# Optimization experiments

Hardware: AMD Instinct MI355X
Metric: run time of the kernel (lower is better)

## Reference

```python
import jax, jax.numpy as jnp
import numpy as np

C, H, K, G = 256, 8, 32, 8
HD = C // H
SCALE = HD ** -0.5
POS_BND = int(0.8 * K * 1 ** 0.5)  # 25
RPE_NUM = 2 * POS_BND + 1          # 51
NW = 4096


def setup_inputs() -> dict:
    key = jax.random.key(0)
    ks = jax.random.split(key, 8)
    data = jax.random.normal(ks[0], (NW * (K + G), C), dtype=jnp.float32)
    # relative xyz offsets between points in a window; exercise the clamp
    rel_pos = jax.random.randint(ks[1], (NW, K, K, 3), -POS_BND - 5, POS_BND + 6).astype(jnp.int32)
    # additive mask: 0 for valid pairs, -100 for masked (padded) pairs
    keep = jax.random.bernoulli(ks[2], 0.9, (NW, K + G, K + G))
    mask = jnp.where(keep, 0.0, -100.0).astype(jnp.float32)
    qkv_w = jax.random.normal(ks[3], (C, 3 * C), dtype=jnp.float32) * (C ** -0.5)
    qkv_b = jnp.zeros((3 * C,), dtype=jnp.float32)
    proj_w = jax.random.normal(ks[4], (C, C), dtype=jnp.float32) * (C ** -0.5)
    proj_b = jnp.zeros((C,), dtype=jnp.float32)
    rpe_table = jax.random.normal(ks[5], (3 * RPE_NUM, H), dtype=jnp.float32) * 0.02
    return {"data": data, "rel_pos": rel_pos, "mask": mask, "qkv_w": qkv_w,
            "qkv_b": qkv_b, "proj_w": proj_w, "proj_b": proj_b, "rpe_table": rpe_table}


def reference(data, rel_pos, mask, qkv_w, qkv_b, proj_w, proj_b, rpe_table):
    W = K + G  # window size including context tokens
    qkv = data @ qkv_w + qkv_b                              # (T, 3C)
    qkv_std = jnp.std(qkv, axis=0, ddof=1)                  # torch .std is unbiased
    qkv = qkv.reshape(-1, W, 3, H, HD).transpose(2, 0, 3, 1, 4)  # (3, Nw, H, W, HD)
    q, k, v = qkv[0] * SCALE, qkv[1], qkv[2]
    attn = jnp.einsum('nhqd,nhkd->nhqk', q, k)              # (Nw, H, W, W)
    # RPE: clamp offsets, index per-axis slices of table, sum over xyz
    idx = jnp.clip(rel_pos, -POS_BND, POS_BND) + POS_BND + jnp.arange(3, dtype=rel_pos.dtype) * RPE_NUM
    rpe = rpe_table[idx].sum(axis=3)                        # (Nw, K, K, H)
    rpe = rpe.transpose(0, 3, 1, 2)                         # (Nw, H, K, K)
    rpe = jnp.pad(rpe, ((0, 0), (0, 0), (G, 0), (G, 0)))    # pad for context tokens
    attn = attn + rpe + mask[:, None]
    attn = jax.nn.softmax(attn, axis=-1)
    out = jnp.einsum('nhqk,nhkd->nqhd', attn, v).reshape(-1, W, C)
    out = out @ proj_w + proj_b                             # (Nw, W, C)
    return (out, qkv_std)
```

## Files before the change

kernel.cpp:

```cpp
#include <hip/hip_runtime.h>
#include <math.h>

#define SCALE_F 0.17677669529663687f

typedef __bf16 bf16x8 __attribute__((ext_vector_type(8)));
typedef float f32x4 __attribute__((ext_vector_type(4)));

__device__ __forceinline__ unsigned short f2bf(float f) {
  unsigned u = __builtin_bit_cast(unsigned, f);
  u = (u + 0x7FFFu + ((u >> 16) & 1u)) >> 16;
  return (unsigned short)u;
}
__device__ __forceinline__ float bf2f(unsigned short u) {
  return __builtin_bit_cast(float, (unsigned)u << 16);
}
__device__ __forceinline__ unsigned pk2(float a, float b) {
  return (unsigned)f2bf(a) | ((unsigned)f2bf(b) << 16);
}
__device__ __forceinline__ bf16x8 ld16(const void* p) {
  int4 v = *(const int4*)p;
  return __builtin_bit_cast(bf16x8, v);
}
__device__ __forceinline__ void gll16(const void* g, void* l) {
  __builtin_amdgcn_global_load_lds(
      (const __attribute__((address_space(1))) unsigned int*)g,
      (__attribute__((address_space(3))) unsigned int*)l, 16, 0, 0);
}


__global__ void octa_prep2(const float* __restrict__ qkv_w, const float* __restrict__ proj_w,
                           unsigned short* __restrict__ wTq, unsigned short* __restrict__ pTq)
{
  int e = blockIdx.x * 256 + threadIdx.x;
  if (e < 196608) {
    int c = e >> 13;
    int nc = c >> 3, kc = c & 7;
    int p2 = e & 8191;
    int n = p2 >> 5, cw = p2 & 31;
    int kl = cw ^ (((n >> 1) & 3) << 3);
    wTq[e] = f2bf(qkv_w[(size_t)(kc * 32 + kl) * 768 + nc * 256 + n]);
  } else {
    int e2 = e - 196608;
    int kc = e2 >> 13, p2 = e2 & 8191;
    int n = p2 >> 5, cw = p2 & 31;
    int kl = cw ^ (((n >> 1) & 3) << 3);
    pTq[e2] = f2bf(proj_w[(size_t)(kc * 32 + kl) * 256 + n]);
  }
}

#define KQ_A0 0
#define KQ_A1 8192
#define KQ_B0 16384
#define KQ_B1 32768
#define KQ_LDS 49152

__global__ __launch_bounds__(512, 4)
void octa_qkv(const float* __restrict__ data, const float* __restrict__ qkv_b,
              const unsigned short* __restrict__ wTq, float* __restrict__ ws,
              char* __restrict__ qg, char* __restrict__ kg, char* __restrict__ vg)
{
  extern __shared__ char smem[];
  const int tid = threadIdx.x, lane = tid & 63, wid = tid >> 6;
  const int ql = lane & 15, lg = lane >> 4;
  const int bm = blockIdx.x / 3, nc = blockIdx.x - bm * 3;
  const int wr = wid >> 2, wc = wid & 3;
  const char* wbase = (const char*)wTq + (size_t)nc * 131072;

  const int arow = tid >> 2, aq = tid & 3;
  const float* abase = data + ((size_t)bm * 128 + arow) * 256 + aq * 8;
  const int alds = arow * 64 + ((aq * 16) ^ (((arow >> 1) & 3) << 4));

  float4 a0 = *(const float4*)abase;
  float4 a1 = *(const float4*)(abase + 4);
  gll16(wbase + wid * 1024 + lane * 16, smem + KQ_B0 + wid * 1024);
  gll16(wbase + 8192 + wid * 1024 + lane * 16, smem + KQ_B0 + 8192 + wid * 1024);
  *(uint2*)(smem + KQ_A0 + alds) = make_uint2(pk2(a0.x, a0.y), pk2(a0.z, a0.w));
  *(uint2*)(smem + KQ_A0 + alds + 8) = make_uint2(pk2(a1.x, a1.y), pk2(a1.z, a1.w));
  __syncthreads();

  f32x4 acc[4][4];
  #pragma unroll
  for (int m = 0; m < 4; ++m)
    #pragma unroll
    for (int n = 0; n < 4; ++n) acc[m][n] = (f32x4){0.f, 0.f, 0.f, 0.f};

  #pragma unroll
  for (int t = 0; t < 8; ++t) {
    float4 na0, na1;
    if (t < 7) {
      na0 = *(const float4*)(abase + (t + 1) * 32);
      na1 = *(const float4*)(abase + (t + 1) * 32 + 4);
      const char* bsrc = wbase + (size_t)(t + 1) * 16384;
      char* bb1 = smem + (((t + 1) & 1) ? KQ_B1 : KQ_B0);
      gll16(bsrc + wid * 1024 + lane * 16, bb1 + wid * 1024);
      gll16(bsrc + 8192 + wid * 1024 + lane * 16, bb1 + 8192 + wid * 1024);
    }
    const char* ab = smem + ((t & 1) ? KQ_A1 : KQ_A0);
    const char* bb = smem + ((t & 1) ? KQ_B1 : KQ_B0);
    bf16x8 af[4], bf[4];
    #pragma unroll
    for (int mt = 0; mt < 4; ++mt) {
      int row = wr * 64 + mt * 16 + ql;
      af[mt] = ld16(ab + row * 64 + ((lg * 16) ^ (((row >> 1) & 3) << 4)));
    }
    #pragma unroll
    for (int nt = 0; nt < 4; ++nt) {
      int n = wc * 64 + nt * 16 + ql;
      bf[nt] = ld16(bb + n * 64 + ((lg * 16) ^ (((n >> 1) & 3) << 4)));
    }
    #pragma unroll
    for (int nt = 0; nt < 4; ++nt)
      #pragma unroll
      for (int mt = 0; mt < 4; ++mt)
        acc[mt][nt] = __builtin_amdgcn_mfma_f32_16x16x32_bf16(af[mt], bf[nt], acc[mt][nt], 0, 0, 0);
    if (t < 7) {
      char* ab1 = smem + (((t + 1) & 1) ? KQ_A1 : KQ_A0);
      *(uint2*)(ab1 + alds) = make_uint2(pk2(na0.x, na0.y), pk2(na0.z, na0.w));
      *(uint2*)(ab1 + alds + 8) = make_uint2(pk2(na1.x, na1.y), pk2(na1.z, na1.w));
    }
    __syncthreads();
  }

  char* base = nc == 0 ? qg : (nc == 1 ? kg : vg);
  const float cs = (nc == 0) ? SCALE_F : 1.0f;
  #pragma unroll
  for (int nt = 0; nt < 4; ++nt) {
    int col = wc * 64 + nt * 16 + ql;
    int h = col >> 5, d = col & 31;
    float bias = qkv_b[nc * 256 + col];
    float s1 = 0.f, s2 = 0.f;
    #pragma unroll
    for (int mt = 0; mt < 4; ++mt) {
      int tg0 = bm * 128 + wr * 64 + mt * 16 + lg * 4;
      int w = tg0 / 40, tk0 = tg0 - w * 40;
      size_t slice = (size_t)(w * 8 + h) * 2560;
      #pragma unroll
      for (int r = 0; r < 4; ++r) {
        float v = acc[mt][nt][r] + bias;
        s1 += v; s2 += v * v;
        *(unsigned short*)(base + slice + (tk0 + r) * 64 + d * 2) = f2bf(v * cs);
      }
    }
    s1 += __shfl_xor(s1, 16); s1 += __shfl_xor(s1, 32);
    s2 += __shfl_xor(s2, 16); s2 += __shfl_xor(s2, 32);
    if (lg == 0) {
      atomicAdd(ws + nc * 256 + col, s1);
      atomicAdd(ws + 768 + nc * 256 + col, s2);
    }
  }
}

#define F3_LDS 30720

__global__ __launch_bounds__(512, 4)
void octa_attnproj3(const char* __restrict__ qg, const char* __restrict__ kg,
                    const char* __restrict__ vg, const float* __restrict__ maskp,
                    const int* __restrict__ rel_pos, const float* __restrict__ rpe_table,
                    const unsigned short* __restrict__ pTq, const float* __restrict__ proj_b,
                    float* __restrict__ out)
{
  extern __shared__ char smem[];
  const int tid = threadIdx.x, w = blockIdx.x, wid = tid >> 6;
  const int lane = tid & 63, ql = lane & 15, lg = lane >> 4, h = wid;
  const int perm = ql * 64 + lg * 16;
  const char* qb = qg + (size_t)(w * 8 + h) * 2560;
  const char* kb = kg + (size_t)(w * 8 + h) * 2560;
  const char* vb = vg + (size_t)(w * 8 + h) * 2560;

  bf16x8 kf0 = ld16(kb + perm), kf1 = ld16(kb + 1024 + perm), kf2 = ld16(kb + 2048 + perm);
  bf16x8 qf0 = ld16(qb + perm), qf1 = ld16(qb + 1024 + perm), qf2 = ld16(qb + 2048 + perm);
  union U8 { unsigned short u[8]; bf16x8 v; };
  U8 ua, ub, uc, ud;
  #pragma unroll
  for (int j = 0; j < 8; ++j) {
    int tok = lg * 8 + j;
    ua.u[j] = *(const unsigned short*)(vb + tok * 64 + ql * 2);
    ub.u[j] = *(const unsigned short*)(vb + tok * 64 + (16 + ql) * 2);
  }
  if (lg == 0) {
    #pragma unroll
    for (int j = 0; j < 8; ++j) {
      uc.u[j] = *(const unsigned short*)(vb + (32 + j) * 64 + ql * 2);
      ud.u[j] = *(const unsigned short*)(vb + (32 + j) * 64 + (16 + ql) * 2);
    }
  } else {
    #pragma unroll
    for (int j = 0; j < 8; ++j) { uc.u[j] = 0; ud.u[j] = 0; }
  }
  bf16x8 vA = ua.v, vB = ub.v, vC = uc.v, vD = ud.v;

  for (int e = tid; e < 1600; e += 512) {
    int qi = e / 40, kj = e - qi * 40;
    float m = maskp[(size_t)w * 1600 + e];
    float b8[8];
    if (qi >= 8 && kj >= 8) {
      const int* rp = rel_pos + ((size_t)w * 1024 + (qi - 8) * 32 + (kj - 8)) * 3;
      int c0 = rp[0], c1 = rp[1], c2 = rp[2];
      c0 = min(25, max(-25, c0)); c1 = min(25, max(-25, c1)); c2 = min(25, max(-25, c2));
      const float4* r0 = (const float4*)(rpe_table + (c0 + 25) * 8);
      const float4* r1 = (const float4*)(rpe_table + (c1 + 76) * 8);
      const float4* r2 = (const float4*)(rpe_table + (c2 + 127) * 8);
      float4 a0 = r0[0], a1 = r1[0], a2 = r2[0];
      float4 b0 = r0[1], b1 = r1[1], b2 = r2[1];
      b8[0] = m + a0.x + a1.x + a2.x; b8[1] = m + a0.y + a1.y + a2.y;
      b8[2] = m + a0.z + a1.z + a2.z; b8[3] = m + a0.w + a1.w + a2.w;
      b8[4] = m + b0.x + b1.x + b2.x; b8[5] = m + b0.y + b1.y + b2.y;
      b8[6] = m + b0.z + b1.z + b2.z; b8[7] = m + b0.w + b1.w + b2.w;
    } else {
      #pragma unroll
      for (int hh = 0; hh < 8; ++hh) b8[hh] = m;
    }
    #pragma unroll
    for (int hh = 0; hh < 8; ++hh)
      *(unsigned short*)(smem + hh * 3200 + kj * 80 + qi * 2) = f2bf(b8[hh]);
  }

  f32x4 st[9];
  {
    bf16x8 kf[3] = {kf0, kf1, kf2}, qf[3] = {qf0, qf1, qf2};
    __builtin_amdgcn_s_setprio(1);
    #pragma unroll
    for (int a = 0; a < 3; ++a)
      #pragma unroll
      for (int b = 0; b < 3; ++b)
        st[a * 3 + b] = __builtin_amdgcn_mfma_f32_16x16x32_bf16(
            kf[a], qf[b], (f32x4){0.f, 0.f, 0.f, 0.f}, 0, 0, 0);
    __builtin_amdgcn_s_setprio(0);
  }
  __syncthreads();

  const char* bb_ = smem + h * 3200;
  float mx[3] = {-3e38f, -3e38f, -3e38f};
  #pragma unroll
  for (int a = 0; a < 3; ++a) {
    #pragma unroll
    for (int b = 0; b < 3; ++b) {
      #pragma unroll
      for (int r = 0; r < 4; ++r) {
        int kj = a * 16 + lg * 4 + r;
        int qi = b * 16 + ql;
        float s = st[a * 3 + b][r];
        if (kj < 40) {
          if (qi < 40)
            s += bf2f(*(const unsigned short*)(bb_ + kj * 80 + qi * 2));
        } else {
          s = -1e30f;
        }
        st[a * 3 + b][r] = s;
        mx[b] = fmaxf(mx[b], s);
      }
    }
  }
  __syncthreads();

  #pragma unroll
  for (int b = 0; b < 3; ++b) {
    mx[b] = fmaxf(mx[b], __shfl_xor(mx[b], 16));
    mx[b] = fmaxf(mx[b], __shfl_xor(mx[b], 32));
  }
  float sum[3] = {0.f, 0.f, 0.f};
  #pragma unroll
  for (int a = 0; a < 3; ++a)
    #pragma unroll
    for (int b = 0; b < 3; ++b)
      #pragma unroll
      for (int r = 0; r < 4; ++r) {
        float e = __expf(st[a * 3 + b][r] - mx[b]);
        st[a * 3 + b][r] = e;
        sum[b] += e;
      }
  float inv[3];
  #pragma unroll
  for (int b = 0; b < 3; ++b) {
    sum[b] += __shfl_xor(sum[b], 16);
    sum[b] += __shfl_xor(sum[b], 32);
    inv[b] = 1.f / sum[b];
  }

  char* pb_ = smem + wid * 3840;
  f32x4 ot[6];
  #pragma unroll
  for (int i = 0; i < 6; ++i) ot[i] = (f32x4){0.f, 0.f, 0.f, 0.f};

  #pragma unroll
  for (int a = 0; a < 2; ++a)
    #pragma unroll
    for (int b = 0; b < 3; ++b)
      #pragma unroll
      for (int r = 0; r < 4; ++r) {
        int kj = a * 16 + lg * 4 + r, qi = b * 16 + ql;
        *(unsigned short*)(pb_ + qi * 80 + kj * 2) = f2bf(st[a * 3 + b][r] * inv[b]);
      }
  asm volatile("" ::: "memory");
  __builtin_amdgcn_s_setprio(1);
  #pragma unroll
  for (int b = 0; b < 3; ++b) {
    bf16x8 pf = ld16(pb_ + (b * 16 + ql) * 80 + lg * 16);
    ot[b]     = __builtin_amdgcn_mfma_f32_16x16x32_bf16(vA, pf, ot[b], 0, 0, 0);
    ot[3 + b] = __builtin_amdgcn_mfma_f32_16x16x32_bf16(vB, pf, ot[3 + b], 0, 0, 0);
  }
  __builtin_amdgcn_s_setprio(0);
  asm volatile("" ::: "memory");
  #pragma unroll
  for (int b = 0; b < 3; ++b) {
    int qi = b * 16 + ql;
    #pragma unroll
    for (int r = 0; r < 4; ++r)
      *(unsigned short*)(pb_ + qi * 80 + (lg * 4 + r) * 2) = f2bf(st[6 + b][r] * inv[b]);
    *(uint2*)(pb_ + qi * 80 + 32 + lg * 8) = make_uint2(0u, 0u);
  }
  asm volatile("" ::: "memory");
  __builtin_amdgcn_s_setprio(1);
  #pragma unroll
  for (int b = 0; b < 3; ++b) {
    bf16x8 pf = ld16(pb_ + (b * 16 + ql) * 80 + lg * 16);
    ot[b]     = __builtin_amdgcn_mfma_f32_16x16x32_bf16(vC, pf, ot[b], 0, 0, 0);
    ot[3 + b] = __builtin_amdgcn_mfma_f32_16x16x32_bf16(vD, pf, ot[3 + b], 0, 0, 0);
  }
  __builtin_amdgcn_s_setprio(0);

  __syncthreads();
  #pragma unroll
  for (int dm = 0; dm < 2; ++dm)
    #pragma unroll
    for (int b = 0; b < 3; ++b) {
      int qi = b * 16 + ql;
      unsigned u0 = pk2(ot[dm * 3 + b][0], ot[dm * 3 + b][1]);
      unsigned u1 = pk2(ot[dm * 3 + b][2], ot[dm * 3 + b][3]);
      int colb = (h * 32 + dm * 16 + lg * 4) * 2;
      *(uint2*)(smem + qi * 512 + (colb ^ ((qi & 7) << 4))) = make_uint2(u0, u1);
    }
  __syncthreads();

  f32x4 pacc[3][2];
  #pragma unroll
  for (int m = 0; m < 3; ++m)
    #pragma unroll
    for (int n = 0; n < 2; ++n) pacc[m][n] = (f32x4){0.f, 0.f, 0.f, 0.f};
  const int c0 = wid * 32;
  const char* pB = (const char*)pTq;

  #pragma unroll
  for (int t = 0; t < 8; ++t) {
    bf16x8 af[3], bfr[2];
    #pragma unroll
    for (int mt = 0; mt < 3; ++mt) {
      int row = mt * 16 + ql;
      af[mt] = ld16(smem + row * 512 + ((t * 64 + lg * 16) ^ ((row & 7) << 4)));
    }
    #pragma unroll
    for (int nt = 0; nt < 2; ++nt) {
      int n = c0 + nt * 16 + ql;
      bfr[nt] = ld16(pB + (size_t)t * 16384 + n * 64 + ((lg * 16) ^ (((n >> 1) & 3) << 4)));
    }
    __builtin_amdgcn_s_setprio(1);
    #pragma unroll
    for (int nt = 0; nt < 2; ++nt)
      #pragma unroll
      for (int mt = 0; mt < 3; ++mt)
        pacc[mt][nt] = __builtin_amdgcn_mfma_f32_16x16x32_bf16(af[mt], bfr[nt], pacc[mt][nt], 0, 0, 0);
    __builtin_amdgcn_s_setprio(0);
  }

  #pragma unroll
  for (int nt = 0; nt < 2; ++nt) {
    int col = c0 + nt * 16 + ql;
    float pb = proj_b[col];
    #pragma unroll
    for (int mt = 0; mt < 3; ++mt)
      #pragma unroll
      for (int r = 0; r < 4; ++r) {
        int row = mt * 16 + lg * 4 + r;
        if (row < 40)
          out[(size_t)(w * 40 + row) * 256 + col] = pacc[mt][nt][r] + pb;
      }
  }
}

__global__ void octa_std(const float* __restrict__ ws, float* __restrict__ out,
                         int total_rows, size_t off)
{
  int j = blockIdx.x * 256 + threadIdx.x;
  if (j < 768) {
    float s = ws[j], ss = ws[768 + j];
    float T = (float)total_rows;
    float var = (ss - s * s / T) / (T - 1.f);
    out[off + j] = sqrtf(fmaxf(var, 0.f));
  }
}

#define O_RPE 0
#define O_MSK 4896
#define O_IDX 8096
#define O_A   12192
#define O_ATT 36768
#define B1_SZ 49152
#define ATT_STRIDE 11776
#define AK 3840
#define AV 7680
#define B2_S (O_ATT + 94208)
#define B2_A O_ATT
#define LDS_BYTES_V4 163744

__device__ __forceinline__ int a_addr(int row, int byte) {
  return O_A + row * 512 + (byte ^ ((row & 7) << 4));
}
__device__ __forceinline__ int v_addr(int d, int byte) {
  return AV + d * 128 + (byte ^ ((d & 7) << 4));
}

__global__ void octa_prep_v4(const float* __restrict__ qkv_w, const float* __restrict__ proj_w,
                             unsigned short* __restrict__ wTq, unsigned short* __restrict__ pTq)
{
  int idx = blockIdx.x * 256 + threadIdx.x;
  if (idx < 196608) {
    int n = idx >> 8, k = idx & 255;
    wTq[idx] = f2bf(qkv_w[k * 768 + n]);
  } else {
    int i = idx - 196608;
    int n = i >> 8, k = i & 255;
    pTq[i] = f2bf(proj_w[k * 256 + n]);
  }
}

__global__ __launch_bounds__(512, 2)
void octa_main_v4(const float* __restrict__ data, const int* __restrict__ rel_pos,
                  const float* __restrict__ maskp, const float* __restrict__ qkv_b,
                  const float* __restrict__ proj_b, const float* __restrict__ rpe_table,
                  const unsigned short* __restrict__ wTq, const unsigned short* __restrict__ pTq,
                  float* __restrict__ ws, float* __restrict__ out)
{
  extern __shared__ char smem[];
  float* s_rpe = (float*)(smem + O_RPE);
  const int tid = threadIdx.x;
  const int w   = blockIdx.x;
  const int wid = tid >> 6;
  const int lane = tid & 63;
  const int ql = lane & 15;
  const int lg = lane >> 4;
  const int h  = wid;
  const int ab = O_ATT + wid * ATT_STRIDE;

  {
    #pragma unroll
    for (int it = 0; it < 6; ++it) {
      int g = it * 512 + tid;
      int n = g >> 2, slot = g & 3;
      const char* src = (const char*)wTq + (size_t)n * 512 + ((slot * 16) ^ ((n & 3) << 4));
      gll16(src, smem + O_ATT + it * 8192 + wid * 1024);
    }
  }
  for (int f = tid; f < 1224; f += 512) s_rpe[f] = rpe_table[f];
  for (int f = tid; f < 400; f += 512) {
    float4 m4 = ((const float4*)(maskp + (size_t)w * 1600))[f];
    uint2 pk;
    pk.x = pk2(m4.x, m4.y); pk.y = pk2(m4.z, m4.w);
    *(uint2*)(smem + O_MSK + f * 8) = pk;
  }
  for (int p = tid; p < 1024; p += 512) {
    const int* rp = rel_pos + ((size_t)w * 1024 + p) * 3;
    int c0 = rp[0], c1 = rp[1], c2 = rp[2];
    c0 = min(25, max(-25, c0)); c1 = min(25, max(-25, c1)); c2 = min(25, max(-25, c2));
    unsigned pk = (unsigned)(c0 + 25) | ((unsigned)(c1 + 76) << 10) | ((unsigned)(c2 + 127) << 20);
    *(unsigned*)(smem + O_IDX + ((p * 4) ^ (((p >> 5) & 7) << 4))) = pk;
  }
  {
    const float4* src = (const float4*)(data + (size_t)w * 10240);
    for (int f = tid; f < 2560; f += 512) {
      int token = f >> 6, q4 = f & 63;
      float4 d4 = src[f];
      uint2 pk;
      pk.x = pk2(d4.x, d4.y); pk.y = pk2(d4.z, d4.w);
      *(uint2*)(smem + a_addr(token, q4 * 8)) = pk;
    }
    int token = 40 + (tid >> 6), byte = (tid & 63) * 8;
    *(uint2*)(smem + a_addr(token, byte)) = make_uint2(0u, 0u);
  }
  __syncthreads();

  f32x4 acc[18];
  #pragma unroll
  for (int i = 0; i < 18; ++i) acc[i] = (f32x4){0.f, 0.f, 0.f, 0.f};

  for (int t = 0; t < 8; ++t) {
    if (t < 7) {
      int bb = O_ATT + ((t + 1) & 1) * B1_SZ;
      #pragma unroll
      for (int it = 0; it < 6; ++it) {
        int g = it * 512 + tid;
        int n = g >> 2, slot = g & 3;
        const char* src = (const char*)wTq + (size_t)n * 512 + (t + 1) * 64
                          + ((slot * 16) ^ ((n & 3) << 4));
        gll16(src, smem + bb + it * 8192 + wid * 1024);
      }
    }
    const int bb = O_ATT + (t & 1) * B1_SZ;
    bf16x8 af[3];
    #pragma unroll
    for (int mt = 0; mt < 3; ++mt)
      af[mt] = ld16(smem + a_addr(mt * 16 + ql, t * 64 + lg * 16));
    #pragma unroll
    for (int j = 0; j < 6; ++j) {
      int n = ((j >> 1) * 16 + 2 * wid + (j & 1)) * 16 + ql;
      bf16x8 bf = ld16(smem + bb + n * 64 + ((lg * 16) ^ ((n & 3) << 4)));
      #pragma unroll
      for (int mt = 0; mt < 3; ++mt)
        acc[j * 3 + mt] = __builtin_amdgcn_mfma_f32_16x16x32_bf16(af[mt], bf, acc[j * 3 + mt], 0, 0, 0);
    }
    __syncthreads();
  }

  {
    #pragma unroll
    for (int it = 0; it < 4; ++it) {
      int g = it * 512 + tid;
      int n = g >> 3, slot = g & 7;
      const char* src = (const char*)pTq + (size_t)n * 512 + ((slot * 16) ^ ((n & 7) << 4));
      gll16(src, smem + B2_S + it * 8192 + wid * 1024);
    }
  }

  #pragma unroll
  for (int j = 0; j < 6; ++j) {
    int sec = j >> 1;
    int ncol = sec * 256 + 32 * wid + (j & 1) * 16 + ql;
    int d = (j & 1) * 16 + ql;
    float bias = qkv_b[ncol];
    float s1 = 0.f, s2 = 0.f;
    #pragma unroll
    for (int mt = 0; mt < 3; ++mt) {
      #pragma unroll
      for (int r = 0; r < 4; ++r) {
        int token = mt * 16 + lg * 4 + r;
        float v = acc[j * 3 + mt][r] + bias;
        if (token < 40) { s1 += v; s2 += v * v; }
        if (sec == 0)
          *(unsigned short*)(smem + ab + token * 80 + d * 2) = f2bf(v * SCALE_F);
        else if (sec == 1)
          *(unsigned short*)(smem + ab + AK + token * 80 + d * 2) = f2bf(v);
        else
          *(unsigned short*)(smem + ab + v_addr(d, token * 2)) = f2bf(v);
      }
    }
    s1 += __shfl_xor(s1, 16); s1 += __shfl_xor(s1, 32);
    s2 += __shfl_xor(s2, 16); s2 += __shfl_xor(s2, 32);
    if (lg == 0) { atomicAdd(ws + ncol, s1); atomicAdd(ws + 768 + ncol, s2); }
  }
  {
    int zd = lane >> 1;
    int zb = 96 + (lane & 1) * 16;
    *(int4*)(smem + ab + v_addr(zd, zb)) = (int4){0, 0, 0, 0};
  }
  asm volatile("" ::: "memory");

  f32x4 st[9];
  {
    bf16x8 kf[3], qf[3];
    #pragma unroll
    for (int a = 0; a < 3; ++a) kf[a] = ld16(smem + ab + AK + (a * 16 + ql) * 80 + lg * 16);
    #pragma unroll
    for (int b = 0; b < 3; ++b) qf[b] = ld16(smem + ab + (b * 16 + ql) * 80 + lg * 16);
    #pragma unroll
    for (int a = 0; a < 3; ++a)
      #pragma unroll
      for (int b = 0; b < 3; ++b)
        st[a * 3 + b] = __builtin_amdgcn_mfma_f32_16x16x32_bf16(
            kf[a], qf[b], (f32x4){0.f, 0.f, 0.f, 0.f}, 0, 0, 0);
  }

  float mx[3] = {-3e38f, -3e38f, -3e38f};
  #pragma unroll
  for (int a = 0; a < 3; ++a) {
    #pragma unroll
    for (int b = 0; b < 3; ++b) {
      #pragma unroll
      for (int r = 0; r < 4; ++r) {
        int kj = a * 16 + lg * 4 + r;
        int qi = b * 16 + ql;
        float s = st[a * 3 + b][r];
        if (kj < 40) {
          if (qi < 40) {
            s += bf2f(*(const unsigned short*)(smem + O_MSK + (qi * 40 + kj) * 2));
            if (kj >= 8 && qi >= 8) {
              int p = (qi - 8) * 32 + (kj - 8);
              unsigned pk = *(const unsigned*)(smem + O_IDX + ((p * 4) ^ (((p >> 5) & 7) << 4)));
              s += s_rpe[(pk & 1023) * 8 + h] + s_rpe[((pk >> 10) & 1023) * 8 + h]
                 + s_rpe[(pk >> 20) * 8 + h];
            }
          }
        } else {
          s = -1e30f;
        }
        st[a * 3 + b][r] = s;
        mx[b] = fmaxf(mx[b], s);
      }
    }
  }
  #pragma unroll
  for (int b = 0; b < 3; ++b) {
    mx[b] = fmaxf(mx[b], __shfl_xor(mx[b], 16));
    mx[b] = fmaxf(mx[b], __shfl_xor(mx[b], 32));
  }
  float sum[3] = {0.f, 0.f, 0.f};
  #pragma unroll
  for (int a = 0; a < 3; ++a)
    #pragma unroll
    for (int b = 0; b < 3; ++b)
      #pragma unroll
      for (int r = 0; r < 4; ++r) {
        float e = __expf(st[a * 3 + b][r] - mx[b]);
        st[a * 3 + b][r] = e;
        sum[b] += e;
      }
  float inv[3];
  #pragma unroll
  for (int b = 0; b < 3; ++b) {
    sum[b] += __shfl_xor(sum[b], 16);
    sum[b] += __shfl_xor(sum[b], 32);
    inv[b] = 1.f / sum[b];
  }

  f32x4 ot[6];
  #pragma unroll
  for (int i = 0; i < 6; ++i) ot[i] = (f32x4){0.f, 0.f, 0.f, 0.f};

  #pragma unroll
  for (int a = 0; a < 2; ++a)
    #pragma unroll
    for (int b = 0; b < 3; ++b)
      #pragma unroll
      for (int r = 0; r < 4; ++r) {
        int kj = a * 16 + lg * 4 + r, qi = b * 16 + ql;
        *(unsigned short*)(smem + ab + qi * 80 + kj * 2) = f2bf(st[a * 3 + b][r] * inv[b]);
      }
  asm volatile("" ::: "memory");
  {
    bf16x8 vf0 = ld16(smem + ab + v_addr(ql, lg * 16));
    bf16x8 vf1 = ld16(smem + ab + v_addr(16 + ql, lg * 16));
    #pragma unroll
    for (int b = 0; b < 3; ++b) {
      bf16x8 pf = ld16(smem + ab + (b * 16 + ql) * 80 + lg * 16);
      ot[b] = __builtin_amdgcn_mfma_f32_16x16x32_bf16(vf0, pf, ot[b], 0, 0, 0);
      ot[3 + b] = __builtin_amdgcn_mfma_f32_16x16x32_bf16(vf1, pf, ot[3 + b], 0, 0, 0);
    }
  }
  asm volatile("" ::: "memory");
  #pragma unroll
  for (int b = 0; b < 3; ++b) {
    int qi = b * 16 + ql;
    #pragma unroll
    for (int r = 0; r < 4; ++r) {
      int kj = 32 + lg * 4 + r;
      *(unsigned short*)(smem + ab + qi * 80 + (kj - 32) * 2) = f2bf(st[6 + b][r] * inv[b]);
    }
    *(uint2*)(smem + ab + qi * 80 + 32 + lg * 8) = make_uint2(0u, 0u);
  }
  asm volatile("" ::: "memory");
  {
    bf16x8 vf0 = ld16(smem + ab + v_addr(ql, 64 + lg * 16));
    bf16x8 vf1 = ld16(smem + ab + v_addr(16 + ql, 64 + lg * 16));
    #pragma unroll
    for (int b = 0; b < 3; ++b) {
      bf16x8 pf = ld16(smem + ab + (b * 16 + ql) * 80 + lg * 16);
      ot[b] = __builtin_amdgcn_mfma_f32_16x16x32_bf16(vf0, pf, ot[b], 0, 0, 0);
      ot[3 + b] = __builtin_amdgcn_mfma_f32_16x16x32_bf16(vf1, pf, ot[3 + b], 0, 0, 0);
    }
  }
  #pragma unroll
  for (int dm = 0; dm < 2; ++dm)
    #pragma unroll
    for (int b = 0; b < 3; ++b)
      #pragma unroll
      for (int r = 0; r < 4; ++r) {
        int d = dm * 16 + lg * 4 + r;
        int qi = b * 16 + ql;
        *(unsigned short*)(smem + a_addr(qi, (h * 32 + d) * 2)) = f2bf(ot[dm * 3 + b][r]);
      }
  __syncthreads();

  f32x4 oacc[6];
  #pragma unroll
  for (int i = 0; i < 6; ++i) oacc[i] = (f32x4){0.f, 0.f, 0.f, 0.f};

  for (int t = 0; t < 4; ++t) {
    if (t < 3) {
      int bb = ((t + 1) & 1) ? B2_A : B2_S;
      #pragma unroll
      for (int it = 0; it < 4; ++it) {
        int g = it * 512 + tid;
        int n = g >> 3, slot = g & 7;
        const char* src = (const char*)pTq + (size_t)n * 512 + (t + 1) * 128
                          + ((slot * 16) ^ ((n & 7) << 4));
        gll16(src, smem + bb + it * 8192 + wid * 1024);
      }
    }
    const int bb = (t & 1) ? B2_A : B2_S;
    #pragma unroll
    for (int ks = 0; ks < 2; ++ks) {
      bf16x8 af[3];
      #pragma unroll
      for (int mt = 0; mt < 3; ++mt)
        af[mt] = ld16(smem + a_addr(mt * 16 + ql, t * 128 + ks * 64 + lg * 16));
      #pragma unroll
      for (int nt = 0; nt < 2; ++nt) {
        int n = (2 * wid + nt) * 16 + ql;
        bf16x8 bf = ld16(smem + bb + n * 128 + ((ks * 64 + lg * 16) ^ ((n & 7) << 4)));
        #pragma unroll
        for (int mt = 0; mt < 3; ++mt)
          oacc[nt * 3 + mt] = __builtin_amdgcn_mfma_f32_16x16x32_bf16(af[mt], bf, oacc[nt * 3 + mt], 0, 0, 0);
      }
    }
    __syncthreads();
  }

  #pragma unroll
  for (int nt = 0; nt < 2; ++nt) {
    int ncol = (2 * wid + nt) * 16 + ql;
    float pb = proj_b[ncol];
    #pragma unroll
    for (int mt = 0; mt < 3; ++mt)
      #pragma unroll
      for (int r = 0; r < 4; ++r) {
        int token = mt * 16 + lg * 4 + r;
        if (token < 40)
          out[(size_t)w * 10240 + token * 256 + ncol] = oacc[nt * 3 + mt][r] + pb;
      }
  }
}

extern "C" void kernel_launch(void* const* d_in, const int* in_sizes, int n_in,
                              void* d_out, int out_size, void* d_ws, size_t ws_size,
                              hipStream_t stream) {
  const float* data    = (const float*)d_in[0];
  const int*   rel_pos = (const int*)d_in[1];
  const float* maskp   = (const float*)d_in[2];
  const float* qkv_w   = (const float*)d_in[3];
  const float* qkv_b   = (const float*)d_in[4];
  const float* proj_w  = (const float*)d_in[5];
  const float* proj_b  = (const float*)d_in[6];
  const float* rpe_tab = (const float*)d_in[7];
  float* out = (float*)d_out;
  float* ws  = (float*)d_ws;

  const int nw = in_sizes[1] / 3072;
  const int total_rows = nw * 40;
  const size_t std_off = (size_t)nw * 10240;
  const size_t SZ = 83886080ull;

  const size_t WS1 = 530432ull + 3ull * SZ + 4096ull;

  unsigned short* wTq = (unsigned short*)((char*)d_ws + 6144);
  unsigned short* pTq = (unsigned short*)((char*)d_ws + 399360);

  hipMemsetAsync(ws, 0, 6144, stream);

  if (ws_size >= WS1) {
    char* qg = (char*)d_ws + 530432;
    char* kg = qg + SZ;
    char* vg = kg + SZ;
    (void)hipFuncSetAttribute((const void*)octa_attnproj3,
                              hipFuncAttributeMaxDynamicSharedMemorySize, F3_LDS);
    hipLaunchKernelGGL(octa_prep2, dim3(1024), dim3(256), 0, stream, qkv_w, proj_w, wTq, pTq);
    hipLaunchKernelGGL(octa_qkv, dim3(nw * 40 / 128 * 3), dim3(512), KQ_LDS, stream,
                       data, qkv_b, wTq, ws, qg, kg, vg);
    hipLaunchKernelGGL(octa_attnproj3, dim3(nw), dim3(512), F3_LDS, stream,
                       qg, kg, vg, maskp, rel_pos, rpe_tab, pTq, proj_b, out);
    hipLaunchKernelGGL(octa_std, dim3(3), dim3(256), 0, stream, ws, out, total_rows, std_off);
  } else {
    hipLaunchKernelGGL(octa_prep_v4, dim3(1024), dim3(256), 0, stream, qkv_w, proj_w, wTq, pTq);
    (void)hipFuncSetAttribute((const void*)octa_main_v4,
                              hipFuncAttributeMaxDynamicSharedMemorySize, LDS_BYTES_V4);
    hipLaunchKernelGGL(octa_main_v4, dim3(nw), dim3(512), LDS_BYTES_V4, stream,
                       data, rel_pos, maskp, qkv_b, proj_b, rpe_tab, wTq, pTq, ws, out);
    hipLaunchKernelGGL(octa_std, dim3(3), dim3(256), 0, stream, ws, out, total_rows, std_off);
  }
}
```

Measured before the change: 353.4 us.

## Pre-convert input to swizzled bf16 and coalesce QKV epilogue stores via LDS

Adds a pre-pass that converts the fp32 input into a pre-swizzled bf16 tile layout, stored in the output buffer as scratch. The QKV GEMM can then stream A tiles with async global-to-LDS loads instead of loading fp32 through registers and converting inside the loop. The epilogue now stages results in LDS and writes 16-byte vectors to the per-head Q/K/V slices, replacing scattered 2-byte stores. The cost is an extra kernel launch plus an extra write and read of the bf16 copy, and epilogue syncs that serialize the two wave-row halves.

```diff
diff --git a/kernel.cpp b/kernel.cpp
--- a/kernel.cpp
+++ b/kernel.cpp
@@ -48,6 +48,25 @@
   }
 }
 
+__global__ __launch_bounds__(256)
+void octa_dprep(const float* __restrict__ data, char* __restrict__ dbf)
+{
+  int e = blockIdx.x * 256 + threadIdx.x;
+  int bm = e >> 12;
+  int r = e & 4095;
+  int t = r >> 9;
+  int rr = r & 511;
+  int row = rr >> 2, u = rr & 3;
+  int l = u ^ ((row >> 1) & 3);
+  const float* src = data + ((size_t)bm * 128 + row) * 256 + t * 32 + l * 8;
+  float4 x = *(const float4*)src;
+  float4 y = *(const float4*)(src + 4);
+  int4 v;
+  v.x = (int)pk2(x.x, x.y); v.y = (int)pk2(x.z, x.w);
+  v.z = (int)pk2(y.x, y.y); v.w = (int)pk2(y.z, y.w);
+  *(int4*)(dbf + (size_t)e * 16) = v;
+}
+
 #define KQ_A0 0
 #define KQ_A1 8192
 #define KQ_B0 16384
@@ -55,7 +74,7 @@
 #define KQ_LDS 49152
 
 __global__ __launch_bounds__(512, 4)
-void octa_qkv(const float* __restrict__ data, const float* __restrict__ qkv_b,
+void octa_qkv(const char* __restrict__ dbf, const float* __restrict__ qkv_b,
               const unsigned short* __restrict__ wTq, float* __restrict__ ws,
               char* __restrict__ qg, char* __restrict__ kg, char* __restrict__ vg)
 {
@@ -65,17 +84,11 @@
   const int bm = blockIdx.x / 3, nc = blockIdx.x - bm * 3;
   const int wr = wid >> 2, wc = wid & 3;
   const char* wbase = (const char*)wTq + (size_t)nc * 131072;
-
-  const int arow = tid >> 2, aq = tid & 3;
-  const float* abase = data + ((size_t)bm * 128 + arow) * 256 + aq * 8;
-  const int alds = arow * 64 + ((aq * 16) ^ (((arow >> 1) & 3) << 4));
-
-  float4 a0 = *(const float4*)abase;
-  float4 a1 = *(const float4*)(abase + 4);
+  const char* abase = dbf + (size_t)bm * 65536;
+
+  gll16(abase + wid * 1024 + lane * 16, smem + KQ_A0 + wid * 1024);
   gll16(wbase + wid * 1024 + lane * 16, smem + KQ_B0 + wid * 1024);
   gll16(wbase + 8192 + wid * 1024 + lane * 16, smem + KQ_B0 + 8192 + wid * 1024);
-  *(uint2*)(smem + KQ_A0 + alds) = make_uint2(pk2(a0.x, a0.y), pk2(a0.z, a0.w));
-  *(uint2*)(smem + KQ_A0 + alds + 8) = make_uint2(pk2(a1.x, a1.y), pk2(a1.z, a1.w));
   __syncthreads();
 
   f32x4 acc[4][4];
@@ -86,12 +99,11 @@
 
   #pragma unroll
   for (int t = 0; t < 8; ++t) {
-    float4 na0, na1;
     if (t < 7) {
-      na0 = *(const float4*)(abase + (t + 1) * 32);
-      na1 = *(const float4*)(abase + (t + 1) * 32 + 4);
+      char* ab1 = smem + (((t + 1) & 1) ? KQ_A1 : KQ_A0);
+      char* bb1 = smem + (((t + 1) & 1) ? KQ_B1 : KQ_B0);
+      gll16(abase + (size_t)(t + 1) * 8192 + wid * 1024 + lane * 16, ab1 + wid * 1024);
       const char* bsrc = wbase + (size_t)(t + 1) * 16384;
-      char* bb1 = smem + (((t + 1) & 1) ? KQ_B1 : KQ_B0);
       gll16(bsrc + wid * 1024 + lane * 16, bb1 + wid * 1024);
       gll16(bsrc + 8192 + wid * 1024 + lane * 16, bb1 + 8192 + wid * 1024);
     }
@@ -113,40 +125,63 @@
       #pragma unroll
       for (int mt = 0; mt < 4; ++mt)
         acc[mt][nt] = __builtin_amdgcn_mfma_f32_16x16x32_bf16(af[mt], bf[nt], acc[mt][nt], 0, 0, 0);
-    if (t < 7) {
-      char* ab1 = smem + (((t + 1) & 1) ? KQ_A1 : KQ_A0);
-      *(uint2*)(ab1 + alds) = make_uint2(pk2(na0.x, na0.y), pk2(na0.z, na0.w));
-      *(uint2*)(ab1 + alds + 8) = make_uint2(pk2(na1.x, na1.y), pk2(na1.z, na1.w));
-    }
     __syncthreads();
   }
 
-  char* base = nc == 0 ? qg : (nc == 1 ? kg : vg);
-  const float cs = (nc == 0) ? SCALE_F : 1.0f;
+  float bv[4];
+  #pragma unroll
+  for (int nt = 0; nt < 4; ++nt)
+    bv[nt] = qkv_b[nc * 256 + wc * 64 + nt * 16 + ql];
+
   #pragma unroll
   for (int nt = 0; nt < 4; ++nt) {
-    int col = wc * 64 + nt * 16 + ql;
-    int h = col >> 5, d = col & 31;
-    float bias = qkv_b[nc * 256 + col];
     float s1 = 0.f, s2 = 0.f;
     #pragma unroll
-    for (int mt = 0; mt < 4; ++mt) {
-      int tg0 = bm * 128 + wr * 64 + mt * 16 + lg * 4;
-      int w = tg0 / 40, tk0 = tg0 - w * 40;
-      size_t slice = (size_t)(w * 8 + h) * 2560;
-      #pragma unroll
-      for (int r = 0; r < 4; ++r) {
-        float v = acc[mt][nt][r] + bias;
+    for (int mt = 0; mt < 4; ++mt)
+      #pragma unroll
+      for (int r = 0; r < 4; ++r) {
+        float v = acc[mt][nt][r] + bv[nt];
         s1 += v; s2 += v * v;
-        *(unsigned short*)(base + slice + (tk0 + r) * 64 + d * 2) = f2bf(v * cs);
-      }
-    }
+      }
     s1 += __shfl_xor(s1, 16); s1 += __shfl_xor(s1, 32);
     s2 += __shfl_xor(s2, 16); s2 += __shfl_xor(s2, 32);
     if (lg == 0) {
+      int col = wc * 64 + nt * 16 + ql;
       atomicAdd(ws + nc * 256 + col, s1);
       atomicAdd(ws + 768 + nc * 256 + col, s2);
     }
+  }
+
+  char* base = nc == 0 ? qg : (nc == 1 ? kg : vg);
+  const float cs = (nc == 0) ? SCALE_F : 1.0f;
+  #pragma unroll
+  for (int hh = 0; hh < 2; ++hh) {
+    if (wr == hh) {
+      #pragma unroll
+      for (int nt = 0; nt < 4; ++nt) {
+        int col = wc * 64 + nt * 16 + ql;
+        #pragma unroll
+        for (int mt = 0; mt < 4; ++mt)
+          #pragma unroll
+          for (int r = 0; r < 4; ++r) {
+            int lrow = mt * 16 + lg * 4 + r;
+            float v = (acc[mt][nt][r] + bv[nt]) * cs;
+            *(unsigned short*)(smem + lrow * 512 + ((col * 2) ^ ((lrow & 7) << 4))) = f2bf(v);
+          }
+      }
+    }
+    __syncthreads();
+    #pragma unroll
+    for (int it = 0; it < 4; ++it) {
+      int c = it * 512 + tid;
+      int lrow = c >> 5, cu = c & 31;
+      int4 val = *(const int4*)(smem + lrow * 512 + ((cu * 16) ^ ((lrow & 7) << 4)));
+      int gtok = bm * 128 + hh * 64 + lrow;
+      int w = gtok / 40, tk = gtok - w * 40;
+      int h = cu >> 2;
+      *(int4*)(base + (size_t)(w * 8 + h) * 2560 + tk * 64 + (cu & 3) * 16) = val;
+    }
+    __syncthreads();
   }
 }
 
@@ -746,6 +781,7 @@
   const int total_rows = nw * 40;
   const size_t std_off = (size_t)nw * 10240;
   const size_t SZ = 83886080ull;
+  const int nbm = nw * 40 / 128;
 
   const size_t WS1 = 530432ull + 3ull * SZ + 4096ull;
 
@@ -758,11 +794,13 @@
     char* qg = (char*)d_ws + 530432;
     char* kg = qg + SZ;
     char* vg = kg + SZ;
+    char* dbf = (char*)d_out;
     (void)hipFuncSetAttribute((const void*)octa_attnproj3,
                               hipFuncAttributeMaxDynamicSharedMemorySize, F3_LDS);
     hipLaunchKernelGGL(octa_prep2, dim3(1024), dim3(256), 0, stream, qkv_w, proj_w, wTq, pTq);
-    hipLaunchKernelGGL(octa_qkv, dim3(nw * 40 / 128 * 3), dim3(512), KQ_LDS, stream,
-                       data, qkv_b, wTq, ws, qg, kg, vg);
+    hipLaunchKernelGGL(octa_dprep, dim3(nbm * 16), dim3(256), 0, stream, data, dbf);
+    hipLaunchKernelGGL(octa_qkv, dim3(nbm * 3), dim3(512), KQ_LDS, stream,
+                       dbf, qkv_b, wTq, ws, qg, kg, vg);
     hipLaunchKernelGGL(octa_attnproj3, dim3(nw), dim3(512), F3_LDS, stream,
                        qg, kg, vg, maskp, rel_pos, rpe_tab, pTq, proj_b, out);
     hipLaunchKernelGGL(octa_std, dim3(3), dim3(256), 0, stream, ws, out, total_rows, std_off);
```

After: 355.6 us. Within noise of the previous version (+0.6%).
